# Optimization experiments

Measured on AMD Instinct MI355X. Metric: run time of the kernel, lower is better.

The kernel has to match this reference:

```python
import jax, jax.numpy as jnp
import numpy as np

NUM_EMBEDDINGS = 4096
EMBEDDING_DIM = 4096
COMMITMENT_COST = 0.25


def setup_inputs() -> dict:
    key = jax.random.key(0)
    k_in, k_cb = jax.random.split(key)
    inputs = jax.random.normal(k_in, (16, 512, EMBEDDING_DIM), dtype=jnp.float32)
    bound = 1.0 / NUM_EMBEDDINGS
    codebook = jax.random.uniform(
        k_cb, (NUM_EMBEDDINGS, EMBEDDING_DIM), dtype=jnp.float32,
        minval=-bound, maxval=bound)
    return {"inputs": inputs, "codebook": codebook}


def reference(inputs, codebook):
    B, K, D = inputs.shape
    flat = inputs.reshape(-1, D)  # [N, D], N = B*K
    distances = (
        jnp.sum(flat * flat, axis=1, keepdims=True)
        + jnp.sum(codebook * codebook, axis=1)
        - 2.0 * jnp.matmul(flat, codebook.T)
    )  # [N, num_embeddings]
    encoding_indices = jnp.argmin(distances, axis=1)  # [N]
    quantized = codebook[encoding_indices].reshape(B, K, D)

    e_latent_loss = jnp.mean((jax.lax.stop_gradient(quantized) - inputs) ** 2)
    q_latent_loss = jnp.mean((quantized - jax.lax.stop_gradient(inputs)) ** 2)
    loss = q_latent_loss + COMMITMENT_COST * e_latent_loss

    # straight-through estimator
    quantized_st = inputs + jax.lax.stop_gradient(quantized - inputs)

    # perplexity: codebook usage entropy (scatter one-hot == bincount)
    N = flat.shape[0]
    counts = jnp.zeros((NUM_EMBEDDINGS,), jnp.float32).at[encoding_indices].add(1.0)
    avg_probs = counts / N
    perplexity = jnp.exp(-jnp.sum(avg_probs * jnp.log(avg_probs + 1e-10)))

    return quantized_st, loss, perplexity
```

## Files before the change

kernel.cpp:

```cpp
#include <hip/hip_runtime.h>
#include <hip/hip_bf16.h>
#include <stdint.h>

typedef unsigned int u32;
typedef unsigned char u8;
typedef unsigned long long u64;
typedef __attribute__((ext_vector_type(8))) int i32x8;
typedef __attribute__((ext_vector_type(4))) int i32x4;
typedef __attribute__((ext_vector_type(4))) float f32x4;

#define NROWS 8192
#define NCODES 4096
#define DIM 4096
#define BK 128
#define KSTEPS (DIM / BK)
#define BM 256
#define BN 256

#define OFF_A      0UL
#define OFF_B      33554432UL
#define OFF_NORMS  50331648UL
#define OFF_RN     50348032UL
#define OFF_AMIN   50380800UL
#define OFF_COUNTS 50446336UL

__device__ __forceinline__ void stage16(const void* g, void* l) {
  __builtin_amdgcn_global_load_lds(
      (const __attribute__((address_space(1))) u32*)g,
      (__attribute__((address_space(3))) u32*)l, 16, 0, 0);
}

__device__ __forceinline__ u32 f2fp8(float f) {
  u32 u = __float_as_uint(f);
  u32 sign = (u >> 24) & 0x80u;
  u32 mag = u & 0x7FFFFFFFu;
  if (mag > 0x43E00000u) mag = 0x43E00000u;
  u32 b;
  if (mag < 0x3C800000u) {
    b = (u32)__float2int_rn(__uint_as_float(mag) * 512.0f);
  } else {
    u32 m = mag + 0x7FFFFu + ((mag >> 20) & 1u);
    u32 e = (m >> 23) - 127u;
    b = (((e + 7u) << 3) | ((m >> 20) & 7u)) & 0x7Fu;
  }
  return sign | b;
}

__device__ __forceinline__ u32 pack4(float4 v) {
  return f2fp8(v.x) | (f2fp8(v.y) << 8) | (f2fp8(v.z) << 16) | (f2fp8(v.w) << 24);
}

__device__ __forceinline__ float waveRed(float s) {
#pragma unroll
  for (int off = 32; off > 0; off >>= 1) s += __shfl_down(s, off);
  return s;
}

__device__ __forceinline__ i32x8 comb(i32x4 lo, i32x4 hi) {
  i32x8 r;
  r[0] = lo[0]; r[1] = lo[1]; r[2] = lo[2]; r[3] = lo[3];
  r[4] = hi[0]; r[5] = hi[1]; r[6] = hi[2]; r[7] = hi[3];
  return r;
}

__global__ void k_cvtA(const float4* __restrict__ in, u32* __restrict__ outA,
                       float* __restrict__ rn, u64* __restrict__ amin) {
  int r = blockIdx.x;
  if (threadIdx.x == 64) amin[r] = ~0ULL;
  const float4* src = in + (size_t)r * (DIM / 4);
  u32* dst = outA + (size_t)r * (DIM / 4);
  float s = 0.0f;
#pragma unroll
  for (int q = 0; q < 4; ++q) {
    int j = q * 256 + threadIdx.x;
    float4 v = src[j];
    s += v.x * v.x + v.y * v.y + v.z * v.z + v.w * v.w;
    dst[j] = pack4(v);
  }
  s = waveRed(s);
  __shared__ float red[4];
  int wid = threadIdx.x >> 6, lane = threadIdx.x & 63;
  if (lane == 0) red[wid] = s;
  __syncthreads();
  if (threadIdx.x == 0) rn[r] = red[0] + red[1] + red[2] + red[3];
}

__global__ void k_cvtB(const float* __restrict__ cb, u32* __restrict__ Bb,
                       float* __restrict__ norms, u32* __restrict__ counts) {
  int row = blockIdx.x;
  if (threadIdx.x == 64) counts[row] = 0u;
  const float4* src = (const float4*)(cb + (size_t)row * DIM);
  u32* dst = Bb + (size_t)row * (DIM / 4);
  float s = 0.0f;
#pragma unroll
  for (int q = 0; q < 4; ++q) {
    int j = q * 256 + threadIdx.x;
    float4 v = src[j];
    s += v.x * v.x + v.y * v.y + v.z * v.z + v.w * v.w;
    float4 sv;
    sv.x = v.x * 4096.0f; sv.y = v.y * 4096.0f;
    sv.z = v.z * 4096.0f; sv.w = v.w * 4096.0f;
    dst[j] = pack4(sv);
  }
  s = waveRed(s);
  __shared__ float red[4];
  int wid = threadIdx.x >> 6, lane = threadIdx.x & 63;
  if (lane == 0) red[wid] = s;
  __syncthreads();
  if (threadIdx.x == 0) norms[row] = red[0] + red[1] + red[2] + red[3];
}

__launch_bounds__(512, 1)
__global__ void k_gemm_argmin(const u8* __restrict__ A,
                              const u8* __restrict__ B,
                              const float* __restrict__ norms,
                              u64* __restrict__ amin) {
  __shared__ u8 As[2][BM * BK];
  __shared__ u8 Bs[2][BN * BK];

  const int bm = blockIdx.x;
  const int bn = blockIdx.y;

  const int tid = threadIdx.x;
  const int w = tid >> 6;
  const int lane = tid & 63;
  const int wr = w >> 2, wc = w & 3;
  const int g = lane >> 4, c = lane & 15;

  const size_t rowA0 = (size_t)bm * BM;
  const size_t rowB0 = (size_t)bn * BN;

  const int colb = (((tid & 7) ^ ((tid >> 3) & 7)) << 4);
  const int srow = tid >> 3;
  const u8* gA = A + rowA0 * DIM + colb;
  const u8* gB = B + rowB0 * DIM + colb;

  const int colo = (((2 * g) ^ (c & 7)) << 4);

  f32x4 acc[8][4] = {};

#define STAGE(buf, kt_)                                                   \
  {                                                                       \
    _Pragma("unroll") for (int j = 0; j < 4; ++j) {                       \
      int o = j * 8192 + tid * 16;                                        \
      int row = j * 64 + srow;                                            \
      stage16(gA + (size_t)row * DIM + (size_t)(kt_)*BK,                  \
              (char*)As[buf] + o);                                        \
      stage16(gB + (size_t)row * DIM + (size_t)(kt_)*BK,                  \
              (char*)Bs[buf] + o);                                        \
    }                                                                     \
  }

#define COMPUTE(buf)                                                      \
  {                                                                       \
    i32x8 bv[4];                                                          \
    _Pragma("unroll") for (int n = 0; n < 4; ++n) {                       \
      int rown = (wc * 64 + n * 16 + c) * BK;                             \
      bv[n] = comb(*(const i32x4*)&Bs[buf][rown + colo],                  \
                   *(const i32x4*)&Bs[buf][rown + (colo ^ 16)]);          \
    }                                                                     \
    _Pragma("unroll") for (int m = 0; m < 8; ++m) {                       \
      int rowm = (wr * 128 + m * 16 + c) * BK;                            \
      i32x8 af = comb(*(const i32x4*)&As[buf][rowm + colo],               \
                      *(const i32x4*)&As[buf][rowm + (colo ^ 16)]);       \
      _Pragma("unroll") for (int n = 0; n < 4; ++n)                       \
          acc[m][n] = __builtin_amdgcn_mfma_scale_f32_16x16x128_f8f6f4(   \
              af, bv[n], acc[m][n], 0, 0, 0, 0x7F7F7F7F, 0, 0x7F7F7F7F);  \
    }                                                                     \
  }

#define WAIT8_BAR()                                          \
  asm volatile("s_waitcnt vmcnt(8)" ::: "memory");           \
  __builtin_amdgcn_s_barrier();                              \
  __builtin_amdgcn_sched_barrier(0);

  STAGE(0, 0);

#pragma unroll 1
  for (int kt2 = 0; kt2 < 15; ++kt2) {
    STAGE(1, 2 * kt2 + 1);
    WAIT8_BAR();
    COMPUTE(0);
    __builtin_amdgcn_s_barrier();
    STAGE(0, 2 * kt2 + 2);
    WAIT8_BAR();
    COMPUTE(1);
    __builtin_amdgcn_s_barrier();
  }
  STAGE(1, 31);
  WAIT8_BAR();
  COMPUTE(0);
  asm volatile("s_waitcnt vmcnt(0)" ::: "memory");
  __builtin_amdgcn_s_barrier();
  __builtin_amdgcn_sched_barrier(0);
  COMPUTE(1);

#undef STAGE
#undef COMPUTE
#undef WAIT8_BAR

  const int rowBase = bm * BM + wr * 128;
  const int colBase = bn * BN + wc * 64;
  float nr[4];
#pragma unroll
  for (int n = 0; n < 4; ++n) nr[n] = norms[colBase + n * 16 + c];

#pragma unroll
  for (int m = 0; m < 8; ++m) {
#pragma unroll
    for (int j = 0; j < 4; ++j) {
      u64 key = ~0ULL;
#pragma unroll
      for (int n = 0; n < 4; ++n) {
        float d = nr[n] - acc[m][n][j] * 4.8828125e-4f;
        u32 u = __float_as_uint(d);
        u = (u & 0x80000000u) ? ~u : (u | 0x80000000u);
        u64 k2 = ((u64)u << 32) | (u32)(colBase + n * 16 + c);
        if (k2 < key) key = k2;
      }
#pragma unroll
      for (int off = 1; off < 16; off <<= 1) {
        u64 o = __shfl_xor(key, off);
        if (o < key) key = o;
      }
      if (c == 0) atomicMin(&amin[rowBase + m * 16 + g * 4 + j], key);
    }
  }
}

__global__ void k_out(const float4* __restrict__ cb, const u64* __restrict__ amin,
                      float4* __restrict__ out, u32* __restrict__ counts) {
  int r = blockIdx.x;
  u32 idx = (u32)(amin[r] & 0xFFFFFFFFu);
  if (threadIdx.x == 0) atomicAdd(&counts[idx], 1u);
  const float4* crow = cb + (size_t)idx * (DIM / 4);
  float4* orow = out + (size_t)r * (DIM / 4);
#pragma unroll
  for (int q = 0; q < 4; ++q) {
    int j = q * 256 + threadIdx.x;
    orow[j] = crow[j];
  }
}

__global__ void k_final(const u32* __restrict__ counts, const u64* __restrict__ amin,
                        const float* __restrict__ rn, float* __restrict__ out) {
  float acc = 0.0f;
  for (int r = threadIdx.x; r < NROWS; r += 256) {
    u32 u = (u32)(amin[r] >> 32);
    u32 b = (u & 0x80000000u) ? (u & 0x7FFFFFFFu) : ~u;
    acc += __uint_as_float(b) + rn[r];
  }
  float ent = 0.0f;
  for (int i = threadIdx.x; i < NCODES; i += 256) {
    float p = (float)counts[i] * (1.0f / (float)NROWS);
    ent -= p * logf(p + 1e-10f);
  }
  acc = waveRed(acc);
  ent = waveRed(ent);
  __shared__ float ra[4], re[4];
  int wid = threadIdx.x >> 6, lane = threadIdx.x & 63;
  if (lane == 0) { ra[wid] = acc; re[wid] = ent; }
  __syncthreads();
  if (threadIdx.x == 0) {
    float sse = ra[0] + ra[1] + ra[2] + ra[3];
    float e = re[0] + re[1] + re[2] + re[3];
    out[(size_t)NROWS * DIM] = 1.25f * sse * (1.0f / (float)((size_t)NROWS * DIM));
    out[(size_t)NROWS * DIM + 1] = expf(e);
  }
}

extern "C" void kernel_launch(void* const* d_in, const int* in_sizes, int n_in,
                              void* d_out, int out_size, void* d_ws, size_t ws_size,
                              hipStream_t stream) {
  const float* d_inputs = (const float*)d_in[0];
  const float* d_cb = (const float*)d_in[1];
  float* out = (float*)d_out;
  char* ws = (char*)d_ws;

  u8* A = (u8*)(ws + OFF_A);
  u8* B = (u8*)(ws + OFF_B);
  float* norms = (float*)(ws + OFF_NORMS);
  float* rn = (float*)(ws + OFF_RN);
  u64* amin = (u64*)(ws + OFF_AMIN);
  u32* counts = (u32*)(ws + OFF_COUNTS);

  k_cvtA<<<NROWS, 256, 0, stream>>>((const float4*)d_inputs, (u32*)A, rn, amin);
  k_cvtB<<<NCODES, 256, 0, stream>>>(d_cb, (u32*)B, norms, counts);
  dim3 grid(NROWS / BM, NCODES / BN);
  k_gemm_argmin<<<grid, 512, 0, stream>>>(A, B, norms, amin);
  k_out<<<NROWS, 256, 0, stream>>>((const float4*)d_cb, amin, (float4*)out, counts);
  k_final<<<1, 256, 0, stream>>>(counts, amin, rn, out);
}
```

Baseline: 267.4 us.

## Restructure FP8 GEMM main loop into ping-pong phases with barriers and setprio

Replaces the per-tile compute block with four phases. Each phase loads two A fragments from LDS, waits on LDS, and runs eight MFMAs under raised wave priority, with barriers around each phase. The next tile's global-to-LDS staging is issued after the first LDS reads of the current tile, and the loop now waits for all outstanding vector memory at the end of each tile instead of keeping eight loads in flight. The goal is to interleave LDS reads, global loads and MFMAs across waves in a ping-pong schedule. The cost is more barriers and the full vmcnt(0) drain, which could expose memory latency.

```diff
diff --git a/kernel.cpp b/kernel.cpp
--- a/kernel.cpp
+++ b/kernel.cpp
@@ -139,6 +139,9 @@
 
   f32x4 acc[8][4] = {};
 
+#define RDB(arr, row) comb(*(const i32x4*)&arr[(row)*BK + colo],          \
+                           *(const i32x4*)&arr[(row)*BK + (colo ^ 16)])
+
 #define STAGE(buf, kt_)                                                   \
   {                                                                       \
     _Pragma("unroll") for (int j = 0; j < 4; ++j) {                       \
@@ -151,53 +154,72 @@
     }                                                                     \
   }
 
-#define COMPUTE(buf)                                                      \
+#define MF(a, b_, cc) __builtin_amdgcn_mfma_scale_f32_16x16x128_f8f6f4(   \
+    a, b_, cc, 0, 0, 0, 0x7F7F7F7F, 0, 0x7F7F7F7F)
+
+#define PHTAIL(m0, m1)                                                    \
+    __builtin_amdgcn_s_barrier();                                         \
+    asm volatile("s_waitcnt lgkmcnt(0)" ::: "memory");                    \
+    __builtin_amdgcn_sched_barrier(0);                                    \
+    __builtin_amdgcn_s_setprio(1);                                        \
+    acc[m0][0] = MF(a0, bv0, acc[m0][0]);                                 \
+    acc[m0][1] = MF(a0, bv1, acc[m0][1]);                                 \
+    acc[m0][2] = MF(a0, bv2, acc[m0][2]);                                 \
+    acc[m0][3] = MF(a0, bv3, acc[m0][3]);                                 \
+    acc[m1][0] = MF(a1, bv0, acc[m1][0]);                                 \
+    acc[m1][1] = MF(a1, bv1, acc[m1][1]);                                 \
+    acc[m1][2] = MF(a1, bv2, acc[m1][2]);                                 \
+    acc[m1][3] = MF(a1, bv3, acc[m1][3]);                                 \
+    __builtin_amdgcn_s_setprio(0);                                        \
+    __builtin_amdgcn_s_barrier();
+
+#define TILE(b, stg, kt_)                                                 \
   {                                                                       \
-    i32x8 bv[4];                                                          \
-    _Pragma("unroll") for (int n = 0; n < 4; ++n) {                       \
-      int rown = (wc * 64 + n * 16 + c) * BK;                             \
-      bv[n] = comb(*(const i32x4*)&Bs[buf][rown + colo],                  \
-                   *(const i32x4*)&Bs[buf][rown + (colo ^ 16)]);          \
-    }                                                                     \
-    _Pragma("unroll") for (int m = 0; m < 8; ++m) {                       \
-      int rowm = (wr * 128 + m * 16 + c) * BK;                            \
-      i32x8 af = comb(*(const i32x4*)&As[buf][rowm + colo],               \
-                      *(const i32x4*)&As[buf][rowm + (colo ^ 16)]);       \
-      _Pragma("unroll") for (int n = 0; n < 4; ++n)                       \
-          acc[m][n] = __builtin_amdgcn_mfma_scale_f32_16x16x128_f8f6f4(   \
-              af, bv[n], acc[m][n], 0, 0, 0, 0x7F7F7F7F, 0, 0x7F7F7F7F);  \
-    }                                                                     \
-  }
-
-#define WAIT8_BAR()                                          \
-  asm volatile("s_waitcnt vmcnt(8)" ::: "memory");           \
-  __builtin_amdgcn_s_barrier();                              \
+    i32x8 bv0, bv1, bv2, bv3, a0, a1;                                     \
+    bv0 = RDB(Bs[b], wc * 64 + 0 + c);                                    \
+    bv1 = RDB(Bs[b], wc * 64 + 16 + c);                                   \
+    bv2 = RDB(Bs[b], wc * 64 + 32 + c);                                   \
+    bv3 = RDB(Bs[b], wc * 64 + 48 + c);                                   \
+    a0 = RDB(As[b], wr * 128 + 0 + c);                                    \
+    a1 = RDB(As[b], wr * 128 + 16 + c);                                   \
+    if (stg) STAGE(b ^ 1, kt_);                                           \
+    PHTAIL(0, 1)                                                          \
+    a0 = RDB(As[b], wr * 128 + 32 + c);                                   \
+    a1 = RDB(As[b], wr * 128 + 48 + c);                                   \
+    PHTAIL(2, 3)                                                          \
+    a0 = RDB(As[b], wr * 128 + 64 + c);                                   \
+    a1 = RDB(As[b], wr * 128 + 80 + c);                                   \
+    PHTAIL(4, 5)                                                          \
+    a0 = RDB(As[b], wr * 128 + 96 + c);                                   \
+    a1 = RDB(As[b], wr * 128 + 112 + c);                                  \
+    PHTAIL(6, 7)                                                          \
+  }
+
+#define VM0BAR()                                                          \
+  asm volatile("s_waitcnt vmcnt(0)" ::: "memory");                        \
+  __builtin_amdgcn_s_barrier();                                           \
   __builtin_amdgcn_sched_barrier(0);
 
   STAGE(0, 0);
+  VM0BAR();
 
 #pragma unroll 1
   for (int kt2 = 0; kt2 < 15; ++kt2) {
-    STAGE(1, 2 * kt2 + 1);
-    WAIT8_BAR();
-    COMPUTE(0);
-    __builtin_amdgcn_s_barrier();
-    STAGE(0, 2 * kt2 + 2);
-    WAIT8_BAR();
-    COMPUTE(1);
-    __builtin_amdgcn_s_barrier();
-  }
-  STAGE(1, 31);
-  WAIT8_BAR();
-  COMPUTE(0);
-  asm volatile("s_waitcnt vmcnt(0)" ::: "memory");
-  __builtin_amdgcn_s_barrier();
-  __builtin_amdgcn_sched_barrier(0);
-  COMPUTE(1);
-
+    TILE(0, 1, 2 * kt2 + 1);
+    VM0BAR();
+    TILE(1, 1, 2 * kt2 + 2);
+    VM0BAR();
+  }
+  TILE(0, 1, 31);
+  VM0BAR();
+  TILE(1, 0, 0);
+
+#undef RDB
 #undef STAGE
-#undef COMPUTE
-#undef WAIT8_BAR
+#undef MF
+#undef PHTAIL
+#undef TILE
+#undef VM0BAR
 
   const int rowBase = bm * BM + wr * 128;
   const int colBase = bn * BN + wc * 64;
```

Measured after the change: 304.6 us. 13.9% more time.
